# Kernel optimization log

Hardware: AMD Instinct MI355X
Metric: run time of the kernel (lower is better)

Reference implementation:

```python
import jax, jax.numpy as jnp
import numpy as np

B, D, INNER, OUT = 8192, 256, 64, 256


def setup_inputs() -> dict:
    key = jax.random.key(0)
    ks = jax.random.split(key, 10)
    s = 0.1
    return {
        "x": jax.random.normal(ks[0], (B, D), dtype=jnp.float32),
        # per-feature inner MLPs: Linear(1, inner) -> ReLU -> Linear(inner, 1)
        "w1": jax.random.normal(ks[1], (D, INNER), dtype=jnp.float32) * s,
        "b1": jax.random.normal(ks[2], (D, INNER), dtype=jnp.float32) * s,
        "w2": jax.random.normal(ks[3], (D, INNER), dtype=jnp.float32) * s,
        "b2": jax.random.normal(ks[4], (D,), dtype=jnp.float32) * s,
        # outer MLP: Linear(D, inner) -> ReLU -> Linear(inner, out)
        "wo1": jax.random.normal(ks[5], (INNER, D), dtype=jnp.float32) * s,
        "bo1": jax.random.normal(ks[6], (INNER,), dtype=jnp.float32) * s,
        "wo2": jax.random.normal(ks[7], (OUT, INNER), dtype=jnp.float32) * s,
        "bo2": jax.random.normal(ks[8], (OUT,), dtype=jnp.float32) * s,
    }


def reference(x, w1, b1, w2, b2, wo1, bo1, wo2, bo2):
    # Vectorized per-feature tiny MLPs: h[b,d,i] = relu(x[b,d]*w1[d,i] + b1[d,i])
    h = jax.nn.relu(x[:, :, None] * w1[None, :, :] + b1[None, :, :])  # [B, D, INNER]
    inner = jnp.einsum('bdi,di->bd', h, w2) + b2[None, :]             # [B, D]
    # Outer MLP
    g = jax.nn.relu(inner @ wo1.T + bo1)                              # [B, INNER]
    return g @ wo2.T + bo2                                            # [B, OUT]
```

## Files before the change

### kernel.cpp

```cpp
#include <hip/hip_runtime.h>
#include <hip/hip_bf16.h>


#define B_TOT 8192
#define D_DIM 256
#define I_DIM 64
#define O_DIM 256
#define RB 16
#define NT 512

typedef __hip_bfloat16 bf16;
using short8 = __attribute__((ext_vector_type(8))) short;
using f32x4  = __attribute__((ext_vector_type(4))) float;


static __device__ __forceinline__ unsigned short f2bf(float v) {
    bf16 h = __float2bfloat16(v);
    return *(unsigned short*)&h;
}

__global__ __launch_bounds__(256)
void kal_prep(const float* __restrict__ w1, const float* __restrict__ b1,
              const float* __restrict__ w2, const float* __restrict__ wo1,
              const float* __restrict__ wo2, void* __restrict__ ws) {
    int idx = blockIdx.x * 256 + threadIdx.x;
    if (idx < 16384) {
        int i = idx >> 8;
        int d = idx & 255;
        ushort4 v;
        v.x = f2bf(w1[d * I_DIM + i]);
        v.y = f2bf(b1[d * I_DIM + i]);
        v.z = f2bf(w2[d * I_DIM + i]);
        v.w = 0;
        ((ushort4*)ws)[idx] = v;
    } else if (idx < 32768) {
        int r   = idx - 16384;
        int kc  = r >> 11;
        int rem = r & 2047;
        int j   = rem >> 5;
        int kk  = rem & 31;
        unsigned short* pbB = (unsigned short*)((char*)ws + 131072);
        pbB[r] = f2bf(wo1[j * D_DIM + kc * 32 + kk]);
    } else if (idx < 49152) {
        int r   = idx - 32768;
        int kc  = r >> 13;
        int rem = r & 8191;
        int o   = rem >> 5;
        int kk  = rem & 31;
        unsigned short* pcB = (unsigned short*)((char*)ws + 163840);
        pcB[r] = f2bf(wo2[o * I_DIM + kc * 32 + kk]);
    }
}

__global__ __launch_bounds__(NT)
void kal_main(const float* __restrict__ x,  const float* __restrict__ b2,
              const float* __restrict__ bo1, const float* __restrict__ bo2,
              const void* __restrict__ ws, float* __restrict__ out) {
    const ushort4* pa  = (const ushort4*)ws;
    const bf16*    pbB = (const bf16*)((const char*)ws + 131072);
    const bf16*    pcB = (const bf16*)((const char*)ws + 163840);

    __shared__ bf16 inner_bf[RB][264];
    __shared__ bf16 g_bf[RB][72];

    const int t    = threadIdx.x;
    const int row0 = blockIdx.x * RB;

    {
        const int d    = t & 255;
        const int half = t >> 8;
        float xv[8], acc[8];
        const float b2v = b2[d];
        #pragma unroll
        for (int b = 0; b < 8; ++b) {
            xv[b]  = x[(row0 + half * 8 + b) * D_DIM + d];
            acc[b] = b2v;
        }
        #pragma unroll 8
        for (int i = 0; i < I_DIM; ++i) {
            const ushort4 wq = pa[i * D_DIM + d];
            const float w1v = __uint_as_float((unsigned)wq.x << 16);
            const float b1v = __uint_as_float((unsigned)wq.y << 16);
            const float w2v = __uint_as_float((unsigned)wq.z << 16);
            #pragma unroll
            for (int b = 0; b < 8; ++b) {
                float h = fmaf(xv[b], w1v, b1v);
                h = fmaxf(h, 0.0f);
                acc[b] = fmaf(h, w2v, acc[b]);
            }
        }
        #pragma unroll
        for (int b = 0; b < 8; ++b)
            inner_bf[half * 8 + b][d] = __float2bfloat16(acc[b]);
    }
    __syncthreads();

    const int lane = t & 63;
    const int wave = t >> 6;
    const int col  = lane & 15;
    const int quad = lane >> 4;

    if (wave < 4) {
        const int j0 = wave * 16;
        f32x4 acc = {0.f, 0.f, 0.f, 0.f};
        #pragma unroll
        for (int kc = 0; kc < 8; ++kc) {
            short8 af = *(const short8*)&inner_bf[col][kc * 32 + quad * 8];
            short8 bfr = *(const short8*)&pbB[(kc * 64 + j0 + col) * 32 + quad * 8];
            acc = __builtin_amdgcn_mfma_f32_16x16x32_bf16(af, bfr, acc, 0, 0, 0);
        }
        const float bo1v = bo1[j0 + col];
        #pragma unroll
        for (int r = 0; r < 4; ++r) {
            const int row = quad * 4 + r;
            g_bf[row][j0 + col] = __float2bfloat16(fmaxf(acc[r] + bo1v, 0.0f));
        }
    }
    __syncthreads();

    #pragma unroll
    for (int tile = 0; tile < 2; ++tile) {
        const int o0 = wave * 16 + tile * 128;
        f32x4 acc = {0.f, 0.f, 0.f, 0.f};
        #pragma unroll
        for (int kc = 0; kc < 2; ++kc) {
            short8 af = *(const short8*)&g_bf[col][kc * 32 + quad * 8];
            short8 bfr = *(const short8*)&pcB[(kc * 256 + o0 + col) * 32 + quad * 8];
            acc = __builtin_amdgcn_mfma_f32_16x16x32_bf16(af, bfr, acc, 0, 0, 0);
        }
        const float bo2v = bo2[o0 + col];
        #pragma unroll
        for (int r = 0; r < 4; ++r)
            out[(row0 + quad * 4 + r) * O_DIM + o0 + col] = acc[r] + bo2v;
    }
}

extern "C" void kernel_launch(void* const* d_in, const int* in_sizes, int n_in,
                              void* d_out, int out_size, void* d_ws, size_t ws_size,
                              hipStream_t stream) {
    const float* x   = (const float*)d_in[0];
    const float* w1  = (const float*)d_in[1];
    const float* b1  = (const float*)d_in[2];
    const float* w2  = (const float*)d_in[3];
    const float* b2  = (const float*)d_in[4];
    const float* wo1 = (const float*)d_in[5];
    const float* bo1 = (const float*)d_in[6];
    const float* wo2 = (const float*)d_in[7];
    const float* bo2 = (const float*)d_in[8];
    float* out = (float*)d_out;

    kal_prep<<<(49152 + 255) / 256, 256, 0, stream>>>(w1, b1, w2, wo1, wo2, d_ws);
    kal_main<<<B_TOT / RB, NT, 0, stream>>>(x, b2, bo1, bo2, d_ws, out);
}
```

Baseline: 90.47 us.

## Halve rows per block and pack two inner-MLP weight sets per 16-byte load

Each block now handles 8 batch rows instead of 16, so the grid doubles to 1024 blocks. The MFMA tiles stay 16 rows, with the upper 8 rows zero-padded in LDS and their output stores masked. The per-feature weights are repacked so one uint4 load brings w1, b1 and w2 for two inner indices, which halves the number of global loads per element and frees the padding slot. Launch bounds now request higher occupancy. In exchange, half of each MFMA's work is wasted on padding rows, and the packed weight stream is reread twice as often across the batch.

Measured after the change: 91.64 us. Within noise of the previous version (+1.3%).

```diff
diff --git a/kernel.cpp b/kernel.cpp
--- a/kernel.cpp
+++ b/kernel.cpp
@@ -6,7 +6,7 @@
 #define D_DIM 256
 #define I_DIM 64
 #define O_DIM 256
-#define RB 16
+#define RB 8
 #define NT 512
 
 typedef __hip_bfloat16 bf16;
@@ -14,9 +14,9 @@
 using f32x4  = __attribute__((ext_vector_type(4))) float;
 
 
-static __device__ __forceinline__ unsigned short f2bf(float v) {
+static __device__ __forceinline__ unsigned f2bfu(float v) {
     bf16 h = __float2bfloat16(v);
-    return *(unsigned short*)&h;
+    return (unsigned)*(unsigned short*)&h;
 }
 
 __global__ __launch_bounds__(256)
@@ -24,74 +24,89 @@
               const float* __restrict__ w2, const float* __restrict__ wo1,
               const float* __restrict__ wo2, void* __restrict__ ws) {
     int idx = blockIdx.x * 256 + threadIdx.x;
-    if (idx < 16384) {
-        int i = idx >> 8;
-        int d = idx & 255;
-        ushort4 v;
-        v.x = f2bf(w1[d * I_DIM + i]);
-        v.y = f2bf(b1[d * I_DIM + i]);
-        v.z = f2bf(w2[d * I_DIM + i]);
+    if (idx < 8192) {
+        int i2 = idx >> 8;
+        int d  = idx & 255;
+        int i  = 2 * i2;
+        uint4 v;
+        v.x = f2bfu(w1[d * I_DIM + i])     | (f2bfu(b1[d * I_DIM + i]) << 16);
+        v.y = f2bfu(w2[d * I_DIM + i])     | (f2bfu(w1[d * I_DIM + i + 1]) << 16);
+        v.z = f2bfu(b1[d * I_DIM + i + 1]) | (f2bfu(w2[d * I_DIM + i + 1]) << 16);
         v.w = 0;
-        ((ushort4*)ws)[idx] = v;
-    } else if (idx < 32768) {
-        int r   = idx - 16384;
+        ((uint4*)ws)[idx] = v;
+    } else if (idx < 24576) {
+        int r   = idx - 8192;
         int kc  = r >> 11;
         int rem = r & 2047;
         int j   = rem >> 5;
         int kk  = rem & 31;
         unsigned short* pbB = (unsigned short*)((char*)ws + 131072);
-        pbB[r] = f2bf(wo1[j * D_DIM + kc * 32 + kk]);
-    } else if (idx < 49152) {
-        int r   = idx - 32768;
+        pbB[r] = (unsigned short)f2bfu(wo1[j * D_DIM + kc * 32 + kk]);
+    } else if (idx < 40960) {
+        int r   = idx - 24576;
         int kc  = r >> 13;
         int rem = r & 8191;
         int o   = rem >> 5;
         int kk  = rem & 31;
         unsigned short* pcB = (unsigned short*)((char*)ws + 163840);
-        pcB[r] = f2bf(wo2[o * I_DIM + kc * 32 + kk]);
+        pcB[r] = (unsigned short)f2bfu(wo2[o * I_DIM + kc * 32 + kk]);
     }
 }
 
-__global__ __launch_bounds__(NT)
+__global__ __launch_bounds__(NT, 8)
 void kal_main(const float* __restrict__ x,  const float* __restrict__ b2,
               const float* __restrict__ bo1, const float* __restrict__ bo2,
               const void* __restrict__ ws, float* __restrict__ out) {
-    const ushort4* pa  = (const ushort4*)ws;
-    const bf16*    pbB = (const bf16*)((const char*)ws + 131072);
-    const bf16*    pcB = (const bf16*)((const char*)ws + 163840);
+    const uint4* pa2 = (const uint4*)ws;
+    const bf16*  pbB = (const bf16*)((const char*)ws + 131072);
+    const bf16*  pcB = (const bf16*)((const char*)ws + 163840);
 
-    __shared__ bf16 inner_bf[RB][264];
-    __shared__ bf16 g_bf[RB][72];
+    __shared__ bf16 inner_bf[16][264];
+    __shared__ bf16 g_bf[16][72];
 
     const int t    = threadIdx.x;
     const int row0 = blockIdx.x * RB;
 
     {
+        bf16 z = __float2bfloat16(0.0f);
+        if (t < 264) {
+            #pragma unroll
+            for (int r = 8; r < 16; ++r) inner_bf[r][t] = z;
+        }
+    }
+
+    {
         const int d    = t & 255;
         const int half = t >> 8;
-        float xv[8], acc[8];
+        float xv[4], acc[4];
         const float b2v = b2[d];
         #pragma unroll
-        for (int b = 0; b < 8; ++b) {
-            xv[b]  = x[(row0 + half * 8 + b) * D_DIM + d];
+        for (int b = 0; b < 4; ++b) {
+            xv[b]  = x[(row0 + half * 4 + b) * D_DIM + d];
             acc[b] = b2v;
         }
-        #pragma unroll 8
-        for (int i = 0; i < I_DIM; ++i) {
-            const ushort4 wq = pa[i * D_DIM + d];
-            const float w1v = __uint_as_float((unsigned)wq.x << 16);
-            const float b1v = __uint_as_float((unsigned)wq.y << 16);
-            const float w2v = __uint_as_float((unsigned)wq.z << 16);
+        #pragma unroll 4
+        for (int i2 = 0; i2 < I_DIM / 2; ++i2) {
+            const uint4 wq = pa2[i2 * D_DIM + d];
+            const float w1a = __uint_as_float(wq.x << 16);
+            const float b1a = __uint_as_float(wq.x & 0xffff0000u);
+            const float w2a = __uint_as_float(wq.y << 16);
+            const float w1b = __uint_as_float(wq.y & 0xffff0000u);
+            const float b1b = __uint_as_float(wq.z << 16);
+            const float w2b = __uint_as_float(wq.z & 0xffff0000u);
             #pragma unroll
-            for (int b = 0; b < 8; ++b) {
-                float h = fmaf(xv[b], w1v, b1v);
-                h = fmaxf(h, 0.0f);
-                acc[b] = fmaf(h, w2v, acc[b]);
+            for (int b = 0; b < 4; ++b) {
+                float ha = fmaf(xv[b], w1a, b1a);
+                ha = fmaxf(ha, 0.0f);
+                acc[b] = fmaf(ha, w2a, acc[b]);
+                float hb = fmaf(xv[b], w1b, b1b);
+                hb = fmaxf(hb, 0.0f);
+                acc[b] = fmaf(hb, w2b, acc[b]);
             }
         }
         #pragma unroll
-        for (int b = 0; b < 8; ++b)
-            inner_bf[half * 8 + b][d] = __float2bfloat16(acc[b]);
+        for (int b = 0; b < 4; ++b)
+            inner_bf[half * 4 + b][d] = __float2bfloat16(acc[b]);
     }
     __syncthreads();
 
@@ -105,7 +120,7 @@
         f32x4 acc = {0.f, 0.f, 0.f, 0.f};
         #pragma unroll
         for (int kc = 0; kc < 8; ++kc) {
-            short8 af = *(const short8*)&inner_bf[col][kc * 32 + quad * 8];
+            short8 af  = *(const short8*)&inner_bf[col][kc * 32 + quad * 8];
             short8 bfr = *(const short8*)&pbB[(kc * 64 + j0 + col) * 32 + quad * 8];
             acc = __builtin_amdgcn_mfma_f32_16x16x32_bf16(af, bfr, acc, 0, 0, 0);
         }
@@ -124,14 +139,16 @@
         f32x4 acc = {0.f, 0.f, 0.f, 0.f};
         #pragma unroll
         for (int kc = 0; kc < 2; ++kc) {
-            short8 af = *(const short8*)&g_bf[col][kc * 32 + quad * 8];
+            short8 af  = *(const short8*)&g_bf[col][kc * 32 + quad * 8];
             short8 bfr = *(const short8*)&pcB[(kc * 256 + o0 + col) * 32 + quad * 8];
             acc = __builtin_amdgcn_mfma_f32_16x16x32_bf16(af, bfr, acc, 0, 0, 0);
         }
-        const float bo2v = bo2[o0 + col];
-        #pragma unroll
-        for (int r = 0; r < 4; ++r)
-            out[(row0 + quad * 4 + r) * O_DIM + o0 + col] = acc[r] + bo2v;
+        if (quad < 2) {
+            const float bo2v = bo2[o0 + col];
+            #pragma unroll
+            for (int r = 0; r < 4; ++r)
+                out[(row0 + quad * 4 + r) * O_DIM + o0 + col] = acc[r] + bo2v;
+        }
     }
 }
 
@@ -149,6 +166,6 @@
     const float* bo2 = (const float*)d_in[8];
     float* out = (float*)d_out;
 
-    kal_prep<<<(49152 + 255) / 256, 256, 0, stream>>>(w1, b1, w2, wo1, wo2, d_ws);
+    kal_prep<<<(40960 + 255) / 256, 256, 0, stream>>>(w1, b1, w2, wo1, wo2, d_ws);
     kal_main<<<B_TOT / RB, NT, 0, stream>>>(x, b2, bo1, bo2, d_ws, out);
 }
```
